# Kernel tuning notes

Hardware: AMD Instinct MI355X
Metric: run time of the kernel (lower is better)

The kernel has to match this reference:

```python
import jax, jax.numpy as jnp
import numpy as np

N = 50000
E = 1600000
F_IN = 4
F_OUT = 32
PERIODS = 12


def setup_inputs() -> dict:
    key = jax.random.key(0)
    ks = jax.random.split(key, 18)
    s_in = 1.0 / np.sqrt(F_IN)
    s_cat = 1.0 / np.sqrt(2 * F_OUT)
    s_out = 1.0 / np.sqrt(F_OUT)
    inp = {
        'x': jax.random.normal(ks[0], (N, F_IN, PERIODS), dtype=jnp.float32),
        'edge_index': jax.random.randint(ks[1], (2, E), 0, N, dtype=jnp.int32),
        'attention': jax.random.uniform(ks[2], (PERIODS,), dtype=jnp.float32),
        # GRU update gate z: GCNConv weight/bias + Linear(2*F_OUT -> F_OUT)
        'Wz': jax.random.normal(ks[3], (F_IN, F_OUT), jnp.float32) * s_in,
        'bz': jnp.zeros((F_OUT,), jnp.float32),
        'Lz': jax.random.normal(ks[4], (2 * F_OUT, F_OUT), jnp.float32) * s_cat,
        'lz': jnp.zeros((F_OUT,), jnp.float32),
        # reset gate r
        'Wr': jax.random.normal(ks[5], (F_IN, F_OUT), jnp.float32) * s_in,
        'br': jnp.zeros((F_OUT,), jnp.float32),
        'Lr': jax.random.normal(ks[6], (2 * F_OUT, F_OUT), jnp.float32) * s_cat,
        'lr': jnp.zeros((F_OUT,), jnp.float32),
        # candidate h
        'Wh': jax.random.normal(ks[7], (F_IN, F_OUT), jnp.float32) * s_in,
        'bh': jnp.zeros((F_OUT,), jnp.float32),
        'Lh': jax.random.normal(ks[8], (2 * F_OUT, F_OUT), jnp.float32) * s_cat,
        'lh': jnp.zeros((F_OUT,), jnp.float32),
        # outer Linear(32 -> periods)
        'Wo': jax.random.normal(ks[9], (F_OUT, PERIODS), jnp.float32) * s_out,
        'bo': jnp.zeros((PERIODS,), jnp.float32),
    }
    return inp


def reference(x, edge_index, attention, Wz, bz, Lz, lz, Wr, br, Lr, lr, Wh, bh, Lh, lh, Wo, bo):
    n = x.shape[0]
    # gcn_norm: add self loops, symmetric D^-1/2 (A+I) D^-1/2
    loop = jnp.arange(n, dtype=edge_index.dtype)
    row = jnp.concatenate([edge_index[0], loop])  # source
    col = jnp.concatenate([edge_index[1], loop])  # target
    w = jnp.ones(row.shape[0], dtype=x.dtype)
    deg = jax.ops.segment_sum(w, col, num_segments=n)
    dinv = jnp.where(deg > 0, jax.lax.rsqrt(deg), 0.0)
    norm = dinv[row] * dinv[col]  # [E+N]

    def conv(xt, W, b):
        h = xt @ W                                   # [N, F_OUT]
        msg = h[row] * norm[:, None]                 # gather + scale
        return jax.ops.segment_sum(msg, col, num_segments=n) + b

    H0 = jnp.zeros((n, F_OUT), dtype=x.dtype)  # A3TGCN passes H=None each period

    def tgcn(xt):
        Z = jax.nn.sigmoid(jnp.concatenate([conv(xt, Wz, bz), H0], axis=1) @ Lz + lz)
        R = jax.nn.sigmoid(jnp.concatenate([conv(xt, Wr, br), H0], axis=1) @ Lr + lr)
        Ht = jnp.tanh(jnp.concatenate([conv(xt, Wh, bh), H0 * R], axis=1) @ Lh + lh)
        return Z * H0 + (1.0 - Z) * Ht

    Hs = jax.vmap(tgcn)(jnp.moveaxis(x, 2, 0))       # [T, N, F_OUT]
    probs = jax.nn.softmax(attention)
    H = jnp.einsum('tnc,t->nc', Hs, probs)           # attention-weighted sum over periods
    return jax.nn.relu(H) @ Wo + bo                  # [N, PERIODS]
```

## Files before the change

### kernel.cpp

```cpp
#include <hip/hip_runtime.h>
#include <hip/hip_fp16.h>
#include <math.h>

#define CHUNK 6144
#define CAPG  10240
#define GNODES 21

union U2H { uint2 u; __half2 h[2]; };

__global__ void k_pre(const float* __restrict__ Wz, const float* __restrict__ Lz, const float* __restrict__ lz,
                      const float* __restrict__ Wh, const float* __restrict__ Lh, const float* __restrict__ lh,
                      const float* __restrict__ bz, const float* __restrict__ bh,
                      const float* __restrict__ att,
                      float* __restrict__ AzT, float* __restrict__ AhT,
                      float* __restrict__ bzp, float* __restrict__ bhp, float* __restrict__ probs,
                      int* __restrict__ gcur) {
  int t = threadIdx.x;
  gcur[t] = 0;
  if (t < 128) {
    int f = t >> 2, k = t & 3;
    float s = 0.f, s2 = 0.f;
    for (int j = 0; j < 32; ++j) {
      s  = fmaf(Wz[k * 32 + j], Lz[j * 32 + f], s);
      s2 = fmaf(Wh[k * 32 + j], Lh[j * 32 + f], s2);
    }
    AzT[t] = s; AhT[t] = s2;
  }
  if (t >= 128 && t < 160) {
    int f = t - 128;
    float s = lz[f], s2 = lh[f];
    for (int j = 0; j < 32; ++j) {
      s  = fmaf(bz[j], Lz[j * 32 + f], s);
      s2 = fmaf(bh[j], Lh[j * 32 + f], s2);
    }
    bzp[f] = s; bhp[f] = s2;
  }
  if (t == 160) {
    float m = att[0];
    for (int i = 1; i < 12; ++i) m = fmaxf(m, att[i]);
    float e[12]; float s = 0.f;
    for (int i = 0; i < 12; ++i) { e[i] = __expf(att[i] - m); s += e[i]; }
    for (int i = 0; i < 12; ++i) probs[i] = e[i] / s;
  }
}

__global__ __launch_bounds__(1024) void k_part(const int* __restrict__ row, const int* __restrict__ col,
                                               int E, int nbkt,
                                               int* __restrict__ gcur, unsigned* __restrict__ part) {
  __shared__ unsigned spak[CHUNK];
  __shared__ unsigned char sbkt[CHUNK];
  __shared__ unsigned char slc[CHUNK];
  __shared__ int hist[256], sscan[256], scur[256], gbase[256];
  int t = threadIdx.x;
  int base = blockIdx.x * CHUNK;
  int cnt = E - base; if (cnt > CHUNK) cnt = CHUNK;
  if (t < 256) hist[t] = 0;
  __syncthreads();
  for (int i = t; i < cnt; i += 1024) {
    int c = col[base + i];
    int b = c >> 8;
    sbkt[i] = (unsigned char)b;
    slc[i]  = (unsigned char)(c & 255);
    atomicAdd(&hist[b], 1);
  }
  __syncthreads();
  int v = 0;
  if (t < 256) { v = hist[t]; sscan[t] = v; }
  __syncthreads();
  for (int off = 1; off < 256; off <<= 1) {
    int a = 0;
    if (t < 256 && t >= off) a = sscan[t - off];
    __syncthreads();
    if (t < 256) sscan[t] += a;
    __syncthreads();
  }
  if (t < 256) {
    sscan[t] -= v;
    gbase[t] = (v > 0) ? atomicAdd(&gcur[t], v) : 0;
    scur[t] = 0;
  }
  __syncthreads();
  for (int i = t; i < cnt; i += 1024) {
    int r = row[base + i];
    int b = sbkt[i];
    int pos = atomicAdd(&scur[b], 1);
    spak[sscan[b] + pos] = ((unsigned)r << 8) | (unsigned)slc[i];
  }
  __syncthreads();
  int wave = t >> 6, lane = t & 63;
  for (int b = wave; b < nbkt; b += 16) {
    int len = hist[b], gb = gbase[b], src = sscan[b];
    int lim = CAPG - gb; if (lim > len) lim = len;
    unsigned* dst = part + (size_t)b * CAPG + gb;
    for (int j = lane; j < lim; j += 64) dst[j] = spak[src + j];
  }
}

__global__ __launch_bounds__(1024) void k_sort(const unsigned* __restrict__ part, const int* __restrict__ gcur,
                                               const float4* __restrict__ x4,
                                               int* __restrict__ csr, int2* __restrict__ rng,
                                               float* __restrict__ dinv, uint2* __restrict__ xh2, int n) {
  __shared__ unsigned sedge[CAPG];
  __shared__ int hist[256], soff[256], scur2[256];
  __shared__ float sdi[256];
  int b = blockIdx.x, t = threadIdx.x;
  int cnt = gcur[b]; if (cnt > CAPG) cnt = CAPG;
  const unsigned* src = part + (size_t)b * CAPG;
  if (t < 256) hist[t] = 0;
  __syncthreads();
  for (int i = t; i < cnt; i += 1024) {
    unsigned e = src[i];
    sedge[i] = e;
    atomicAdd(&hist[e & 255u], 1);
  }
  __syncthreads();
  int v = 0;
  if (t < 256) { v = hist[t]; soff[t] = v; }
  __syncthreads();
  for (int off = 1; off < 256; off <<= 1) {
    int a = 0;
    if (t < 256 && t >= off) a = soff[t - off];
    __syncthreads();
    if (t < 256) soff[t] += a;
    __syncthreads();
  }
  int base = b * CAPG;
  if (t < 256) {
    int excl = soff[t] - v;
    int node = b * 256 + t;
    float di = rsqrtf((float)(v + 1));
    sdi[t] = di;
    if (node < n) {
      rng[node] = make_int2(base + excl, base + excl + v);
      dinv[node] = di;
    }
    soff[t] = excl;
    scur2[t] = 0;
  }
  __syncthreads();
  for (int i = t; i < cnt; i += 1024) {
    unsigned e = sedge[i];
    int lc = (int)(e & 255u);
    int pos = atomicAdd(&scur2[lc], 1);
    csr[base + soff[lc] + pos] = (int)(e >> 8);
  }
  int gb = b * 3072;
  for (int j = t; j < 3072; j += 1024) {
    int gi = gb + j;
    if (gi < n * 12) {
      float4 f = x4[gi];
      float d = sdi[j / 12];
      __half2 h0 = __floats2half2_rn(d * f.x, d * f.y);
      __half2 h1 = __floats2half2_rn(d * f.z, d * f.w);
      uint2 u; u.x = *(unsigned*)&h0; u.y = *(unsigned*)&h1;
      xh2[gi] = u;
    }
  }
}

__global__ __launch_bounds__(256) void k_gather(const int* __restrict__ csr, const int2* __restrict__ rng,
                                                const float* __restrict__ dinv, const uint2* __restrict__ xh2,
                                                const float* __restrict__ AzT, const float* __restrict__ AhT,
                                                const float* __restrict__ bzp, const float* __restrict__ bhp,
                                                const float* __restrict__ probs,
                                                const float* __restrict__ Wo, const float* __restrict__ bo,
                                                float* __restrict__ out, int n) {
  __shared__ float sY[GNODES * 49];
  __shared__ float sH[GNODES * 33];
  __shared__ float4 sAz4[32], sAh4[32];
  __shared__ float sbzp[32], sbhp[32], sprobs[12], sbo[12], sWo[384];
  int t = threadIdx.x;
  int nb = blockIdx.x * GNODES;

  if (t < 32) {
    sAz4[t] = ((const float4*)AzT)[t];
    sAh4[t] = ((const float4*)AhT)[t];
    sbzp[t] = bzp[t]; sbhp[t] = bhp[t];
  }
  if (t >= 32 && t < 44) { sprobs[t - 32] = probs[t - 32]; sbo[t - 32] = bo[t - 32]; }
  for (int i = t; i < 384; i += 256) sWo[i] = Wo[i];

  int grp = t / 12, c = t - grp * 12;
  int node = nb + grp;
  if (grp < GNODES && node < n) {
    U2H s; s.u = xh2[(size_t)node * 12 + c];
    float2 f0 = __half22float2(s.h[0]), f1 = __half22float2(s.h[1]);
    float a0 = f0.x, a1 = f0.y, a2 = f1.x, a3 = f1.y;
    int2 r = rng[node];
    int e = r.x, end = r.y;
#define ACC4(V) { \
    float2 g0 = __half22float2(V.h[0]), g1 = __half22float2(V.h[1]); \
    a0 += g0.x; a1 += g0.y; a2 += g1.x; a3 += g1.y; }
    for (; e + 8 <= end; e += 8) {
      int r0 = csr[e],     r1 = csr[e + 1], r2 = csr[e + 2], r3 = csr[e + 3];
      int r4 = csr[e + 4], r5 = csr[e + 5], r6 = csr[e + 6], r7 = csr[e + 7];
      U2H v0, v1, v2, v3, v4, v5, v6, v7;
      v0.u = xh2[(size_t)r0 * 12 + c];
      v1.u = xh2[(size_t)r1 * 12 + c];
      v2.u = xh2[(size_t)r2 * 12 + c];
      v3.u = xh2[(size_t)r3 * 12 + c];
      v4.u = xh2[(size_t)r4 * 12 + c];
      v5.u = xh2[(size_t)r5 * 12 + c];
      v6.u = xh2[(size_t)r6 * 12 + c];
      v7.u = xh2[(size_t)r7 * 12 + c];
      ACC4(v0) ACC4(v1) ACC4(v2) ACC4(v3) ACC4(v4) ACC4(v5) ACC4(v6) ACC4(v7)
    }
    for (; e < end; ++e) {
      int r0 = csr[e];
      U2H v0; v0.u = xh2[(size_t)r0 * 12 + c];
      ACC4(v0)
    }
#undef ACC4
    float di = dinv[node];
    float* yb = sY + grp * 49 + c * 4;
    yb[0] = a0 * di; yb[1] = a1 * di; yb[2] = a2 * di; yb[3] = a3 * di;
  }
  __syncthreads();

  for (int u = t; u < GNODES * 32; u += 256) {
    int ln = u >> 5, f = u & 31;
    if (nb + ln >= n) continue;
    const float* y = sY + ln * 49;
    float4 az = sAz4[f], ah = sAh4[f];
    float bzf = sbzp[f], bhf = sbhp[f];
    float acc = 0.f;
#pragma unroll
    for (int tt = 0; tt < 12; ++tt) {
      float y0 = y[tt], y1 = y[12 + tt], y2 = y[24 + tt], y3 = y[36 + tt];
      float za = fmaf(az.x, y0, fmaf(az.y, y1, fmaf(az.z, y2, fmaf(az.w, y3, bzf))));
      float ha = fmaf(ah.x, y0, fmaf(ah.y, y1, fmaf(ah.z, y2, fmaf(ah.w, y3, bhf))));
      float ez = __expf(za);
      float ax = fabsf(ha);
      float e2 = __expf(-2.f * ax);
      float g = (1.f - e2) / ((1.f + ez) * (1.f + e2));
      acc = fmaf(sprobs[tt], copysignf(g, ha), acc);
    }
    sH[ln * 33 + f] = fmaxf(acc, 0.f);
  }
  __syncthreads();

  if (t < GNODES * 12) {
    int ln = t / 12, p = t - ln * 12;
    int node2 = nb + ln;
    if (node2 < n) {
      float acc = sbo[p];
      const float* h = sH + ln * 33;
      const float* wv = sWo + p;
#pragma unroll
      for (int f2 = 0; f2 < 32; ++f2) acc = fmaf(h[f2], wv[f2 * 12], acc);
      out[node2 * 12 + p] = acc;
    }
  }
}

extern "C" void kernel_launch(void* const* d_in, const int* in_sizes, int n_in,
                              void* d_out, int out_size, void* d_ws, size_t ws_size,
                              hipStream_t stream) {
  const float* x   = (const float*)d_in[0];
  const int*   ei  = (const int*)d_in[1];
  const float* att = (const float*)d_in[2];
  const float* Wz  = (const float*)d_in[3];
  const float* bz  = (const float*)d_in[4];
  const float* Lz  = (const float*)d_in[5];
  const float* lz  = (const float*)d_in[6];
  const float* Wh  = (const float*)d_in[11];
  const float* bh  = (const float*)d_in[12];
  const float* Lh  = (const float*)d_in[13];
  const float* lh  = (const float*)d_in[14];
  const float* Wo  = (const float*)d_in[15];
  const float* bo  = (const float*)d_in[16];
  float* out = (float*)d_out;

  const int N = in_sizes[0] / (4 * 12);
  const int E = in_sizes[1] / 2;
  const int NBKT = (N + 255) >> 8;
  const int* row = ei;
  const int* col = ei + E;

  char* w = (char*)d_ws;
  size_t o = 0;
  auto alloc = [&](size_t bytes) -> char* {
    o = (o + 255) & ~(size_t)255;
    char* p = w + o; o += bytes; return p;
  };
  float* pAzT   = (float*)alloc(128 * 4);
  float* pAhT   = (float*)alloc(128 * 4);
  float* pbzp   = (float*)alloc(32 * 4);
  float* pbhp   = (float*)alloc(32 * 4);
  float* pprobs = (float*)alloc(12 * 4);
  int*   pgcur  = (int*)alloc(256 * 4);
  float* pdinv  = (float*)alloc((size_t)NBKT * 256 * 4);
  int2*  prng   = (int2*)alloc((size_t)N * 8);
  unsigned* ppart = (unsigned*)alloc((size_t)256 * CAPG * 4);
  int*   pcsr   = (int*)alloc((size_t)256 * CAPG * 4);
  uint2* pxh    = (uint2*)alloc((size_t)NBKT * 256 * 12 * 8);
  (void)ws_size; (void)n_in; (void)out_size;

  k_pre<<<1, 256, 0, stream>>>(Wz, Lz, lz, Wh, Lh, lh, bz, bh, att,
                               pAzT, pAhT, pbzp, pbhp, pprobs, pgcur);
  k_part<<<(E + CHUNK - 1) / CHUNK, 1024, 0, stream>>>(row, col, E, NBKT, pgcur, ppart);
  k_sort<<<NBKT, 1024, 0, stream>>>(ppart, pgcur, (const float4*)x, pcsr, prng, pdinv, pxh, N);
  k_gather<<<(N + GNODES - 1) / GNODES, 256, 0, stream>>>(pcsr, prng, pdinv, pxh,
                                                          pAzT, pAhT, pbzp, pbhp, pprobs,
                                                          Wo, bo, out, N);
}
```

Measured before the change: 170.0 us.

## Split sort blocks in half, use wave-shuffle scans, and flatten partition scatter

Several changes land together across the preprocessing kernels. The k_part chunk shrinks from 6144 to 4096, its 256-entry scan becomes a wave shuffle scan, and the global write-out is now a flat per-element scatter driven by a stored bucket tag instead of a per-bucket wave copy loop. k_sort launches two blocks per bucket, each handling 128 local nodes with a shuffle scan, and it stores CSR indices premultiplied by 12 so the gather drops one multiply per edge. The gcur reset moves from k_pre to a memset. In exchange, each k_sort half-block re-reads the whole bucket from global memory, and an extra memset call is added to the launch sequence.

```diff
diff --git a/kernel.cpp b/kernel.cpp
--- a/kernel.cpp
+++ b/kernel.cpp
@@ -2,7 +2,7 @@
 #include <hip/hip_fp16.h>
 #include <math.h>
 
-#define CHUNK 6144
+#define CHUNK 4096
 #define CAPG  10240
 #define GNODES 21
 
@@ -13,10 +13,8 @@
                       const float* __restrict__ bz, const float* __restrict__ bh,
                       const float* __restrict__ att,
                       float* __restrict__ AzT, float* __restrict__ AhT,
-                      float* __restrict__ bzp, float* __restrict__ bhp, float* __restrict__ probs,
-                      int* __restrict__ gcur) {
+                      float* __restrict__ bzp, float* __restrict__ bhp, float* __restrict__ probs) {
   int t = threadIdx.x;
-  gcur[t] = 0;
   if (t < 128) {
     int f = t >> 2, k = t & 3;
     float s = 0.f, s2 = 0.f;
@@ -50,7 +48,9 @@
   __shared__ unsigned spak[CHUNK];
   __shared__ unsigned char sbkt[CHUNK];
   __shared__ unsigned char slc[CHUNK];
+  __shared__ unsigned char sdst[CHUNK];
   __shared__ int hist[256], sscan[256], scur[256], gbase[256];
+  __shared__ int swsum[4];
   int t = threadIdx.x;
   int base = blockIdx.x * CHUNK;
   int cnt = E - base; if (cnt > CHUNK) cnt = CHUNK;
@@ -64,35 +64,38 @@
     atomicAdd(&hist[b], 1);
   }
   __syncthreads();
-  int v = 0;
-  if (t < 256) { v = hist[t]; sscan[t] = v; }
-  __syncthreads();
-  for (int off = 1; off < 256; off <<= 1) {
-    int a = 0;
-    if (t < 256 && t >= off) a = sscan[t - off];
-    __syncthreads();
-    if (t < 256) sscan[t] += a;
-    __syncthreads();
-  }
+  int v = 0, sincl = 0;
+  int lane = t & 63, wid = t >> 6;
   if (t < 256) {
-    sscan[t] -= v;
+    v = hist[t];
+    sincl = v;
+    for (int d = 1; d < 64; d <<= 1) {
+      int y = __shfl_up(sincl, d, 64);
+      if (lane >= d) sincl += y;
+    }
+    if (lane == 63) swsum[wid] = sincl;
+  }
+  __syncthreads();
+  if (t < 256) {
+    int wpre = 0;
+    for (int k = 0; k < wid; ++k) wpre += swsum[k];
+    sscan[t] = sincl + wpre - v;
     gbase[t] = (v > 0) ? atomicAdd(&gcur[t], v) : 0;
     scur[t] = 0;
   }
   __syncthreads();
   for (int i = t; i < cnt; i += 1024) {
-    int r = row[base + i];
     int b = sbkt[i];
     int pos = atomicAdd(&scur[b], 1);
-    spak[sscan[b] + pos] = ((unsigned)r << 8) | (unsigned)slc[i];
-  }
-  __syncthreads();
-  int wave = t >> 6, lane = t & 63;
-  for (int b = wave; b < nbkt; b += 16) {
-    int len = hist[b], gb = gbase[b], src = sscan[b];
-    int lim = CAPG - gb; if (lim > len) lim = len;
-    unsigned* dst = part + (size_t)b * CAPG + gb;
-    for (int j = lane; j < lim; j += 64) dst[j] = spak[src + j];
+    int j = sscan[b] + pos;
+    spak[j] = ((unsigned)row[base + i] << 8) | (unsigned)slc[i];
+    sdst[j] = (unsigned char)b;
+  }
+  __syncthreads();
+  for (int i = t; i < cnt; i += 1024) {
+    int b = sdst[i];
+    int gb = gbase[b] + (i - sscan[b]);
+    if (gb < CAPG) part[(size_t)b * CAPG + gb] = spak[i];
   }
 }
 
@@ -101,51 +104,61 @@
                                                int* __restrict__ csr, int2* __restrict__ rng,
                                                float* __restrict__ dinv, uint2* __restrict__ xh2, int n) {
   __shared__ unsigned sedge[CAPG];
-  __shared__ int hist[256], soff[256], scur2[256];
-  __shared__ float sdi[256];
-  int b = blockIdx.x, t = threadIdx.x;
-  int cnt = gcur[b]; if (cnt > CAPG) cnt = CAPG;
-  const unsigned* src = part + (size_t)b * CAPG;
-  if (t < 256) hist[t] = 0;
+  __shared__ int hist[128], soff[128], scur2[128];
+  __shared__ float sdi[128];
+  __shared__ int swsum[2], sbase;
+  int blk = blockIdx.x, t = threadIdx.x;
+  int B = blk >> 1, h = blk & 1;
+  int cnt = gcur[B]; if (cnt > CAPG) cnt = CAPG;
+  const unsigned* src = part + (size_t)B * CAPG;
+  if (t < 128) hist[t] = 0;
   __syncthreads();
   for (int i = t; i < cnt; i += 1024) {
     unsigned e = src[i];
     sedge[i] = e;
-    atomicAdd(&hist[e & 255u], 1);
-  }
-  __syncthreads();
-  int v = 0;
-  if (t < 256) { v = hist[t]; soff[t] = v; }
-  __syncthreads();
-  for (int off = 1; off < 256; off <<= 1) {
-    int a = 0;
-    if (t < 256 && t >= off) a = soff[t - off];
-    __syncthreads();
-    if (t < 256) soff[t] += a;
-    __syncthreads();
-  }
-  int base = b * CAPG;
-  if (t < 256) {
-    int excl = soff[t] - v;
-    int node = b * 256 + t;
+    int lc = (int)(e & 255u);
+    if ((lc >> 7) == h) atomicAdd(&hist[lc & 127], 1);
+  }
+  __syncthreads();
+  int v = 0, sincl = 0;
+  int lane = t & 63, wid = t >> 6;
+  if (t < 128) {
+    v = hist[t];
+    sincl = v;
+    for (int d = 1; d < 64; d <<= 1) {
+      int y = __shfl_up(sincl, d, 64);
+      if (lane >= d) sincl += y;
+    }
+    if (lane == 63) swsum[wid] = sincl;
+  }
+  __syncthreads();
+  if (t < 128) {
+    int wpre = (wid == 1) ? swsum[0] : 0;
+    int excl = sincl + wpre - v;
+    int m1 = swsum[0] + swsum[1];
+    int bb = B * CAPG + (h ? (cnt - m1) : 0);
+    int node = B * 256 + h * 128 + t;
     float di = rsqrtf((float)(v + 1));
     sdi[t] = di;
     if (node < n) {
-      rng[node] = make_int2(base + excl, base + excl + v);
+      rng[node] = make_int2(bb + excl, bb + excl + v);
       dinv[node] = di;
     }
     soff[t] = excl;
     scur2[t] = 0;
+    if (t == 0) sbase = bb;
   }
   __syncthreads();
   for (int i = t; i < cnt; i += 1024) {
     unsigned e = sedge[i];
     int lc = (int)(e & 255u);
-    int pos = atomicAdd(&scur2[lc], 1);
-    csr[base + soff[lc] + pos] = (int)(e >> 8);
-  }
-  int gb = b * 3072;
-  for (int j = t; j < 3072; j += 1024) {
+    if ((lc >> 7) == h) {
+      int pos = atomicAdd(&scur2[lc & 127], 1);
+      csr[sbase + soff[lc & 127] + pos] = (int)(e >> 8) * 12;
+    }
+  }
+  int gb = B * 3072 + h * 1536;
+  for (int j = t; j < 1536; j += 1024) {
     int gi = gb + j;
     if (gi < n * 12) {
       float4 f = x4[gi];
@@ -183,7 +196,8 @@
   int grp = t / 12, c = t - grp * 12;
   int node = nb + grp;
   if (grp < GNODES && node < n) {
-    U2H s; s.u = xh2[(size_t)node * 12 + c];
+    const uint2* xb = xh2 + c;
+    U2H s; s.u = xb[(size_t)node * 12];
     float2 f0 = __half22float2(s.h[0]), f1 = __half22float2(s.h[1]);
     float a0 = f0.x, a1 = f0.y, a2 = f1.x, a3 = f1.y;
     int2 r = rng[node];
@@ -195,19 +209,13 @@
       int r0 = csr[e],     r1 = csr[e + 1], r2 = csr[e + 2], r3 = csr[e + 3];
       int r4 = csr[e + 4], r5 = csr[e + 5], r6 = csr[e + 6], r7 = csr[e + 7];
       U2H v0, v1, v2, v3, v4, v5, v6, v7;
-      v0.u = xh2[(size_t)r0 * 12 + c];
-      v1.u = xh2[(size_t)r1 * 12 + c];
-      v2.u = xh2[(size_t)r2 * 12 + c];
-      v3.u = xh2[(size_t)r3 * 12 + c];
-      v4.u = xh2[(size_t)r4 * 12 + c];
-      v5.u = xh2[(size_t)r5 * 12 + c];
-      v6.u = xh2[(size_t)r6 * 12 + c];
-      v7.u = xh2[(size_t)r7 * 12 + c];
+      v0.u = xb[r0]; v1.u = xb[r1]; v2.u = xb[r2]; v3.u = xb[r3];
+      v4.u = xb[r4]; v5.u = xb[r5]; v6.u = xb[r6]; v7.u = xb[r7];
       ACC4(v0) ACC4(v1) ACC4(v2) ACC4(v3) ACC4(v4) ACC4(v5) ACC4(v6) ACC4(v7)
     }
     for (; e < end; ++e) {
       int r0 = csr[e];
-      U2H v0; v0.u = xh2[(size_t)r0 * 12 + c];
+      U2H v0; v0.u = xb[r0];
       ACC4(v0)
     }
 #undef ACC4
@@ -244,10 +252,10 @@
     int node2 = nb + ln;
     if (node2 < n) {
       float acc = sbo[p];
-      const float* h = sH + ln * 33;
+      const float* hh = sH + ln * 33;
       const float* wv = sWo + p;
 #pragma unroll
-      for (int f2 = 0; f2 < 32; ++f2) acc = fmaf(h[f2], wv[f2 * 12], acc);
+      for (int f2 = 0; f2 < 32; ++f2) acc = fmaf(hh[f2], wv[f2 * 12], acc);
       out[node2 * 12 + p] = acc;
     }
   }
@@ -296,10 +304,11 @@
   uint2* pxh    = (uint2*)alloc((size_t)NBKT * 256 * 12 * 8);
   (void)ws_size; (void)n_in; (void)out_size;
 
+  hipMemsetAsync(pgcur, 0, 256 * 4, stream);
   k_pre<<<1, 256, 0, stream>>>(Wz, Lz, lz, Wh, Lh, lh, bz, bh, att,
-                               pAzT, pAhT, pbzp, pbhp, pprobs, pgcur);
+                               pAzT, pAhT, pbzp, pbhp, pprobs);
   k_part<<<(E + CHUNK - 1) / CHUNK, 1024, 0, stream>>>(row, col, E, NBKT, pgcur, ppart);
-  k_sort<<<NBKT, 1024, 0, stream>>>(ppart, pgcur, (const float4*)x, pcsr, prng, pdinv, pxh, N);
+  k_sort<<<NBKT * 2, 1024, 0, stream>>>(ppart, pgcur, (const float4*)x, pcsr, prng, pdinv, pxh, N);
   k_gather<<<(N + GNODES - 1) / GNODES, 256, 0, stream>>>(pcsr, prng, pdinv, pxh,
                                                           pAzT, pAhT, pbzp, pbhp, pprobs,
                                                           Wo, bo, out, N);
```

Measured after the change: 170.7 us. Within noise of the previous version (+0.4%).
